# Optimization experiments

Hardware: AMD Instinct MI355X
Metric: run time of the kernel (lower is better)

## Reference

```python
import jax, jax.numpy as jnp
import numpy as np

N_NODES = 50000
N_EDGES = 600000
BAG = 16
VOCAB = 10000
EMB = 128
HID = 128
N_CLASSES = 10
N_GRAPHS = 512
PAD_IDX = 1


def setup_inputs() -> dict:
    key = jax.random.key(0)
    ks = jax.random.split(key, 12)
    x_tokens = jax.random.randint(ks[0], (N_NODES, BAG), 0, VOCAB)
    src = jax.random.randint(ks[1], (N_EDGES,), 0, N_NODES)
    dst = jax.random.randint(ks[2], (N_EDGES,), 0, N_NODES)
    edge_index = jnp.stack([src, dst])
    batch = jnp.sort(jax.random.randint(ks[3], (N_NODES,), 0, N_GRAPHS))
    # rows 0,1 are zero in the original (weights[2:] filled from pretrained vectors)
    emb_table = (jax.random.normal(ks[4], (VOCAB, EMB)) * 0.02).at[:2].set(0.0)
    s = 1.0 / np.sqrt(EMB)
    w1_l = jax.random.normal(ks[5], (HID, EMB)) * s
    b1 = jnp.zeros((HID,), jnp.float32)
    w1_r = jax.random.normal(ks[6], (HID, EMB)) * s
    w2_l = jax.random.normal(ks[7], (HID, HID)) * s
    b2 = jnp.zeros((HID,), jnp.float32)
    w2_r = jax.random.normal(ks[8], (HID, HID)) * s
    w_out = jax.random.normal(ks[9], (N_CLASSES, HID)) * s
    b_out = jnp.zeros((N_CLASSES,), jnp.float32)
    return {"x_tokens": x_tokens, "edge_index": edge_index, "batch": batch,
            "emb_table": emb_table, "w1_l": w1_l, "b1": b1, "w1_r": w1_r,
            "w2_l": w2_l, "b2": b2, "w2_r": w2_r, "w_out": w_out, "b_out": b_out}


def _embedding_bag_mean(tokens, table):
    # nn.EmbeddingBag mode='mean' with padding_idx: padding tokens excluded from mean
    emb = table[tokens]                                  # [N, BAG, D]
    mask = (tokens != PAD_IDX)[..., None].astype(table.dtype)
    total = jnp.sum(emb * mask, axis=1)                  # [N, D]
    cnt = jnp.clip(jnp.sum(mask, axis=1), 1.0)           # [N, 1]
    return total / cnt


def _sage_conv(x, src, dst, w_l, b_l, w_r):
    # PyG SAGEConv: lin_l(mean_{j in N(i)} x_j) + lin_r(x_i); lin_r has no bias
    n = x.shape[0]
    msg_sum = jax.ops.segment_sum(x[src], dst, num_segments=n)           # [N, D]
    deg = jax.ops.segment_sum(jnp.ones((src.shape[0], 1), x.dtype), dst,
                              num_segments=n)                             # [N, 1]
    aggr = msg_sum / jnp.clip(deg, 1.0)
    return aggr @ w_l.T + b_l + x @ w_r.T


def reference(x_tokens, edge_index, batch, emb_table, w1_l, b1, w1_r,
              w2_l, b2, w2_r, w_out, b_out):
    src, dst = edge_index[0], edge_index[1]
    x = _embedding_bag_mean(x_tokens, emb_table)                 # [N, EMB]
    x = jax.nn.relu(_sage_conv(x, src, dst, w1_l, b1, w1_r))     # [N, HID]
    x = jax.nn.relu(_sage_conv(x, src, dst, w2_l, b2, w2_r))     # [N, HID]
    # global_mean_pool over graph ids
    g_sum = jax.ops.segment_sum(x, batch, num_segments=N_GRAPHS)
    g_cnt = jax.ops.segment_sum(jnp.ones((x.shape[0], 1), x.dtype), batch,
                                num_segments=N_GRAPHS)
    g = g_sum / jnp.clip(g_cnt, 1.0)                             # [G, HID]
    return g @ w_out.T + b_out                                   # [G, C]
```

## Files before the change

### kernel.cpp

```cpp
#include <hip/hip_runtime.h>
#include <hip/hip_bf16.h>

#define NN 50000
#define NE 600000
#define BAG 16
#define EMB 128
#define HID 128
#define NC 10
#define NG 512
#define PAD_IDX 1
#define VOCAB 10000
#define SLOTS 64
#define TPAIRS (VOCAB * EMB / 2)
#define WPAIRS (4 * HID * EMB / 2)
#define NE8 (NE / 8)
#define SC8BLK ((NE8 + 255) / 256)
#define EMVB (NN / 16)
#define NTILES ((NN + 127) / 128)

typedef __attribute__((ext_vector_type(8))) short v8s;
typedef __attribute__((ext_vector_type(4))) float v4f;

__device__ __forceinline__ float bflo(unsigned u) { return __uint_as_float(u << 16); }
__device__ __forceinline__ float bfhi(unsigned u) { return __uint_as_float(u & 0xffff0000u); }
__device__ __forceinline__ unsigned short f2bf(float f) {
    unsigned u = __float_as_uint(f);
    return (unsigned short)((u + 0x7fffu + ((u >> 16) & 1u)) >> 16);
}
__device__ __forceinline__ void acc8(float* a, v8s v) {
    unsigned* u = (unsigned*)&v;
#pragma unroll
    for (int j = 0; j < 4; j++) {
        a[2 * j] += bflo(u[j]);
        a[2 * j + 1] += bfhi(u[j]);
    }
}

__global__ void k_conv(const float* __restrict__ t, unsigned short* __restrict__ tb,
                       const float* __restrict__ w1l, const float* __restrict__ w1r,
                       const float* __restrict__ w2l, const float* __restrict__ w2r,
                       unsigned short* __restrict__ wbf, int* __restrict__ cnt,
                       float* __restrict__ gsum, float* __restrict__ gcnt) {
    int i = blockIdx.x * blockDim.x + threadIdx.x;
    if (i < NN) cnt[i] = 0;
    if (i < NG * HID) gsum[i] = 0.f;
    if (i < NG) gcnt[i] = 0.f;
    if (i < TPAIRS) {
        float2 v = *(const float2*)(t + (size_t)i * 2);
        unsigned lo = f2bf(v.x), hi = f2bf(v.y);
        *(unsigned*)(tb + (size_t)i * 2) = lo | (hi << 16);
    } else if (i < TPAIRS + WPAIRS) {
        int j = i - TPAIRS;
        int k = j * 2;
        int arr = k >> 14;
        int o = k & 16383;
        const float* w = (arr == 0) ? w1l : (arr == 1) ? w1r : (arr == 2) ? w2l : w2r;
        float2 v = *(const float2*)(w + o);
        unsigned lo = f2bf(v.x), hi = f2bf(v.y);
        *(unsigned*)(wbf + k) = lo | (hi << 16);
    }
}

__global__ __launch_bounds__(256) void k_scatem(const int* __restrict__ src,
                                                const int* __restrict__ dst,
                                                int* __restrict__ cnt,
                                                int* __restrict__ slots,
                                                const int* __restrict__ tokens,
                                                const unsigned short* __restrict__ table,
                                                unsigned short* __restrict__ x0) {
    int b = blockIdx.x;
    if (b < EMVB) {
        int sl = threadIdx.x & 15;
        int node = b * 16 + (threadIdx.x >> 4);
        const int* tp = tokens + node * BAG;
        float a[8];
#pragma unroll
        for (int j = 0; j < 8; j++) a[j] = 0.f;
        int c = 0;
#pragma unroll
        for (int t = 0; t < BAG; t++) {
            int tok = tp[t];
            c += (tok != PAD_IDX);
            v8s v = *(const v8s*)(table + (size_t)tok * EMB + sl * 8);
            acc8(a, v);
        }
        float inv = 1.0f / (float)(c > 0 ? c : 1);
        uint4 o;
        o.x = f2bf(a[0] * inv) | ((unsigned)f2bf(a[1] * inv) << 16);
        o.y = f2bf(a[2] * inv) | ((unsigned)f2bf(a[3] * inv) << 16);
        o.z = f2bf(a[4] * inv) | ((unsigned)f2bf(a[5] * inv) << 16);
        o.w = f2bf(a[6] * inv) | ((unsigned)f2bf(a[7] * inv) << 16);
        *(uint4*)(x0 + (size_t)node * EMB + sl * 8) = o;
        return;
    }
    int t = (b - EMVB) * 256 + threadIdx.x;
    if (t < NE8) {
        int4 s0 = *((const int4*)src + t * 2);
        int4 s1 = *((const int4*)src + t * 2 + 1);
        int4 d0 = *((const int4*)dst + t * 2);
        int4 d1 = *((const int4*)dst + t * 2 + 1);
        int p0 = atomicAdd(&cnt[d0.x], 1);
        int p1 = atomicAdd(&cnt[d0.y], 1);
        int p2 = atomicAdd(&cnt[d0.z], 1);
        int p3 = atomicAdd(&cnt[d0.w], 1);
        int p4 = atomicAdd(&cnt[d1.x], 1);
        int p5 = atomicAdd(&cnt[d1.y], 1);
        int p6 = atomicAdd(&cnt[d1.z], 1);
        int p7 = atomicAdd(&cnt[d1.w], 1);
        if (p0 < SLOTS) slots[(size_t)d0.x * SLOTS + p0] = s0.x;
        if (p1 < SLOTS) slots[(size_t)d0.y * SLOTS + p1] = s0.y;
        if (p2 < SLOTS) slots[(size_t)d0.z * SLOTS + p2] = s0.z;
        if (p3 < SLOTS) slots[(size_t)d0.w * SLOTS + p3] = s0.w;
        if (p4 < SLOTS) slots[(size_t)d1.x * SLOTS + p4] = s1.x;
        if (p5 < SLOTS) slots[(size_t)d1.y * SLOTS + p5] = s1.y;
        if (p6 < SLOTS) slots[(size_t)d1.z * SLOTS + p6] = s1.z;
        if (p7 < SLOTS) slots[(size_t)d1.w * SLOTS + p7] = s1.w;
    }
}

__global__ __launch_bounds__(256) void k_aggr(const unsigned short* __restrict__ x,
                                              const int* __restrict__ cnt,
                                              const int* __restrict__ slots,
                                              unsigned short* __restrict__ aggr) {
    int node = blockIdx.x * 4 + (threadIdx.x >> 6);
    int lane = threadIdx.x & 63;
    if (node >= NN) return;
    int deg = cnt[node];
    int m = deg > SLOTS ? SLOTS : deg;
    int g = lane >> 4, sl = lane & 15;
    float a[8];
#pragma unroll
    for (int j = 0; j < 8; j++) a[j] = 0.f;
    int idx_l = slots[(size_t)node * SLOTS + ((lane < m) ? lane : 0)];
    int i = 0;
    for (; i + 8 <= m; i += 8) {
        int t0 = __shfl(idx_l, i + g, 64);
        int t1 = __shfl(idx_l, i + 4 + g, 64);
        v8s v0 = *(const v8s*)(x + (size_t)t0 * HID + sl * 8);
        v8s v1 = *(const v8s*)(x + (size_t)t1 * HID + sl * 8);
        acc8(a, v0);
        acc8(a, v1);
    }
    for (; i + 4 <= m; i += 4) {
        int t0 = __shfl(idx_l, i + g, 64);
        v8s v0 = *(const v8s*)(x + (size_t)t0 * HID + sl * 8);
        acc8(a, v0);
    }
    int rem = m - i;
    if (rem > 0) {
        int t0 = __shfl(idx_l, (g < rem) ? i + g : i, 64);
        v8s v0 = *(const v8s*)(x + (size_t)t0 * HID + sl * 8);
        if (g < rem) acc8(a, v0);
    }
#pragma unroll
    for (int j = 0; j < 8; j++) {
        a[j] += __shfl_xor(a[j], 16, 64);
        a[j] += __shfl_xor(a[j], 32, 64);
    }
    float inv = 1.0f / (float)(deg > 0 ? deg : 1);
    if (g == 0) {
        uint4 o;
        o.x = f2bf(a[0] * inv) | ((unsigned)f2bf(a[1] * inv) << 16);
        o.y = f2bf(a[2] * inv) | ((unsigned)f2bf(a[3] * inv) << 16);
        o.z = f2bf(a[4] * inv) | ((unsigned)f2bf(a[5] * inv) << 16);
        o.w = f2bf(a[6] * inv) | ((unsigned)f2bf(a[7] * inv) << 16);
        *(uint4*)(aggr + (size_t)node * HID + sl * 8) = o;
    }
}

__device__ __forceinline__ void sage_kloop(int row0, const unsigned short* __restrict__ xa,
                                           const unsigned short* __restrict__ xr,
                                           const unsigned short* __restrict__ wl,
                                           const unsigned short* __restrict__ wr,
                                           unsigned short* As, unsigned short* Bs,
                                           v4f acc[2][8]) {
    int tid = threadIdx.x;
    int wave = tid >> 6, lane = tid & 63;
    int q = lane >> 4, l16 = lane & 15;
    for (int kc = 0; kc < 8; kc++) {
        const unsigned short* Ag = (kc < 4) ? xa : xr;
        const unsigned short* Bg = (kc < 4) ? wl : wr;
        int koff = (kc & 3) * 32;
#pragma unroll
        for (int it = 0; it < 2; it++) {
            int seg = tid + it * 256;
            int r = seg >> 2, sg = seg & 3;
            int gr = row0 + r;
            if (gr > NN - 1) gr = NN - 1;
            v8s a = *(const v8s*)(Ag + (size_t)gr * HID + koff + sg * 8);
            *(v8s*)(As + r * 32 + sg * 8) = a;
            v8s b = *(const v8s*)(Bg + (size_t)r * HID + koff + sg * 8);
            *(v8s*)(Bs + r * 32 + sg * 8) = b;
        }
        __syncthreads();
        v8s a0 = *(const v8s*)(As + (wave * 32 + l16) * 32 + q * 8);
        v8s a1 = *(const v8s*)(As + (wave * 32 + 16 + l16) * 32 + q * 8);
#pragma unroll
        for (int nt = 0; nt < 8; nt++) {
            v8s b = *(const v8s*)(Bs + (nt * 16 + l16) * 32 + q * 8);
            acc[0][nt] = __builtin_amdgcn_mfma_f32_16x16x32_bf16(a0, b, acc[0][nt], 0, 0, 0);
            acc[1][nt] = __builtin_amdgcn_mfma_f32_16x16x32_bf16(a1, b, acc[1][nt], 0, 0, 0);
        }
        __syncthreads();
    }
}

__global__ __launch_bounds__(256) void k_sage(const unsigned short* __restrict__ xa,
                                              const unsigned short* __restrict__ xr,
                                              const unsigned short* __restrict__ wl,
                                              const unsigned short* __restrict__ wr,
                                              const float* __restrict__ bias,
                                              unsigned short* __restrict__ out) {
    __shared__ unsigned short As[128 * 32];
    __shared__ unsigned short Bs[128 * 32];
    int row0 = blockIdx.x * 128;
    v4f acc[2][8];
#pragma unroll
    for (int m = 0; m < 2; m++)
#pragma unroll
        for (int n = 0; n < 8; n++) acc[m][n] = (v4f){0.f, 0.f, 0.f, 0.f};
    sage_kloop(row0, xa, xr, wl, wr, As, Bs, acc);
    int tid = threadIdx.x;
    int wave = tid >> 6, lane = tid & 63;
    int q = lane >> 4, l16 = lane & 15;
#pragma unroll
    for (int nt = 0; nt < 8; nt++) {
        int col = nt * 16 + l16;
        float bv = bias[col];
#pragma unroll
        for (int mt = 0; mt < 2; mt++) {
#pragma unroll
            for (int r = 0; r < 4; r++) {
                int row = row0 + wave * 32 + mt * 16 + q * 4 + r;
                if (row < NN) {
                    float v = acc[mt][nt][r] + bv;
                    v = v > 0.f ? v : 0.f;
                    out[(size_t)row * HID + col] = f2bf(v);
                }
            }
        }
    }
}

__global__ __launch_bounds__(256) void k_sagepool(const unsigned short* __restrict__ xa,
                                                  const unsigned short* __restrict__ xr,
                                                  const unsigned short* __restrict__ wl,
                                                  const unsigned short* __restrict__ wr,
                                                  const float* __restrict__ bias,
                                                  const int* __restrict__ batch,
                                                  float* __restrict__ gsum,
                                                  float* __restrict__ gcnt) {
    __shared__ unsigned short smem[128 * 128];
    unsigned short* As = smem;
    unsigned short* Bs = smem + 128 * 32;
    int row0 = blockIdx.x * 128;
    v4f acc[2][8];
#pragma unroll
    for (int m = 0; m < 2; m++)
#pragma unroll
        for (int n = 0; n < 8; n++) acc[m][n] = (v4f){0.f, 0.f, 0.f, 0.f};
    sage_kloop(row0, xa, xr, wl, wr, As, Bs, acc);
    int tid = threadIdx.x;
    int wave = tid >> 6, lane = tid & 63;
    int q = lane >> 4, l16 = lane & 15;
#pragma unroll
    for (int nt = 0; nt < 8; nt++) {
        int col = nt * 16 + l16;
        float bv = bias[col];
#pragma unroll
        for (int mt = 0; mt < 2; mt++) {
#pragma unroll
            for (int r = 0; r < 4; r++) {
                int rl = wave * 32 + mt * 16 + q * 4 + r;
                float v = acc[mt][nt][r] + bv;
                v = v > 0.f ? v : 0.f;
                smem[rl * 128 + col] = f2bf(v);
            }
        }
    }
    __syncthreads();
    if (tid < 128) {
        int col = tid;
        int end = NN - row0;
        if (end > 128) end = 128;
        int cur = batch[row0];
        float acc_p = 0.f;
        int c = 0;
        for (int i = 0; i < end; i++) {
            int b = batch[row0 + i];
            if (b != cur) {
                atomicAdd(&gsum[cur * HID + col], acc_p);
                if (col == 0) atomicAdd(&gcnt[cur], (float)c);
                acc_p = 0.f;
                c = 0;
                cur = b;
            }
            acc_p += __uint_as_float(((unsigned)smem[i * 128 + col]) << 16);
            c++;
        }
        atomicAdd(&gsum[cur * HID + col], acc_p);
        if (col == 0) atomicAdd(&gcnt[cur], (float)c);
    }
}

__global__ __launch_bounds__(128) void k_final(const float* __restrict__ gsum,
                                               const float* __restrict__ gcnt,
                                               const float* __restrict__ w_out,
                                               const float* __restrict__ b_out,
                                               float* __restrict__ out) {
    __shared__ float mean[HID];
    int g = blockIdx.x, tid = threadIdx.x;
    mean[tid] = gsum[g * HID + tid] / fmaxf(gcnt[g], 1.0f);
    __syncthreads();
    if (tid < NC) {
        float s = b_out[tid];
#pragma unroll 16
        for (int d = 0; d < HID; d++) s += mean[d] * w_out[tid * HID + d];
        out[g * NC + tid] = s;
    }
}

extern "C" void kernel_launch(void* const* d_in, const int* in_sizes, int n_in,
                              void* d_out, int out_size, void* d_ws, size_t ws_size,
                              hipStream_t stream) {
    const int* x_tokens = (const int*)d_in[0];
    const int* edge = (const int*)d_in[1];
    const int* batch = (const int*)d_in[2];
    const float* emb_table = (const float*)d_in[3];
    const float* w1l = (const float*)d_in[4];
    const float* b1 = (const float*)d_in[5];
    const float* w1r = (const float*)d_in[6];
    const float* w2l = (const float*)d_in[7];
    const float* b2 = (const float*)d_in[8];
    const float* w2r = (const float*)d_in[9];
    const float* w_out = (const float*)d_in[10];
    const float* b_out = (const float*)d_in[11];
    float* out = (float*)d_out;

    char* ws = (char*)d_ws;
    size_t off = 0;
    auto alloc = [&](size_t bytes) {
        void* p = ws + off;
        off += (bytes + 255) & ~(size_t)255;
        return p;
    };
    int* cnt = (int*)alloc(NN * 4);
    int* slots = (int*)alloc((size_t)NN * SLOTS * 4);
    unsigned short* wbf = (unsigned short*)alloc(4 * HID * EMB * 2);
    float* gsum = (float*)alloc(NG * HID * 4);
    float* gcnt = (float*)alloc(NG * 4);
    unsigned short* x0 = (unsigned short*)alloc((size_t)NN * EMB * 2);
    unsigned short* x1 = (unsigned short*)alloc((size_t)NN * HID * 2);
    unsigned short* aggrb = (unsigned short*)alloc((size_t)NN * HID * 2);
    unsigned short* table_bf = x1;

    const int* srcp = edge;
    const int* dstp = edge + NE;

    k_conv<<<(TPAIRS + WPAIRS + 255) / 256, 256, 0, stream>>>(
        emb_table, table_bf, w1l, w1r, w2l, w2r, wbf, cnt, gsum, gcnt);
    k_scatem<<<EMVB + SC8BLK, 256, 0, stream>>>(srcp, dstp, cnt, slots, x_tokens,
                                                table_bf, x0);
    k_aggr<<<(NN + 3) / 4, 256, 0, stream>>>(x0, cnt, slots, aggrb);
    k_sage<<<NTILES, 256, 0, stream>>>(aggrb, x0, wbf, wbf + 16384, b1, x1);
    k_aggr<<<(NN + 3) / 4, 256, 0, stream>>>(x1, cnt, slots, aggrb);
    k_sagepool<<<NTILES, 256, 0, stream>>>(aggrb, x1, wbf + 32768, wbf + 49152, b2,
                                           batch, gsum, gcnt);
    k_final<<<NG, 128, 0, stream>>>(gsum, gcnt, w_out, b_out, out);
}
```

Before: 210.7 us.

## Assign 16 threads per node in aggregation instead of a full wave

The neighbor-mean aggregation kernel now maps each node to a 16-lane group, so one 256-thread block handles 16 nodes instead of 4. Each group walks its node's full neighbor list with vectorized int4 index loads and eight independent row gathers per iteration. This removes the cross-group shuffle reduction, the shuffle-based index broadcast and the idle lanes on low-degree nodes. In exchange, lanes within a wave can diverge when node degrees differ, and each thread serially accumulates more rows.

Measured after the change: 213.5 us. Within noise of the previous version (+1.3%).

```diff
diff --git a/kernel.cpp b/kernel.cpp
--- a/kernel.cpp
+++ b/kernel.cpp
@@ -16,6 +16,7 @@
 #define NE8 (NE / 8)
 #define SC8BLK ((NE8 + 255) / 256)
 #define EMVB (NN / 16)
+#define AGVB (NN / 16)
 #define NTILES ((NN + 127) / 128)
 
 typedef __attribute__((ext_vector_type(8))) short v8s;
@@ -122,50 +123,58 @@
                                               const int* __restrict__ cnt,
                                               const int* __restrict__ slots,
                                               unsigned short* __restrict__ aggr) {
-    int node = blockIdx.x * 4 + (threadIdx.x >> 6);
-    int lane = threadIdx.x & 63;
-    if (node >= NN) return;
+    int sl = threadIdx.x & 15;
+    int node = blockIdx.x * 16 + (threadIdx.x >> 4);
     int deg = cnt[node];
     int m = deg > SLOTS ? SLOTS : deg;
-    int g = lane >> 4, sl = lane & 15;
+    const int* srow = slots + (size_t)node * SLOTS;
     float a[8];
 #pragma unroll
     for (int j = 0; j < 8; j++) a[j] = 0.f;
-    int idx_l = slots[(size_t)node * SLOTS + ((lane < m) ? lane : 0)];
-    int i = 0;
-    for (; i + 8 <= m; i += 8) {
-        int t0 = __shfl(idx_l, i + g, 64);
-        int t1 = __shfl(idx_l, i + 4 + g, 64);
-        v8s v0 = *(const v8s*)(x + (size_t)t0 * HID + sl * 8);
-        v8s v1 = *(const v8s*)(x + (size_t)t1 * HID + sl * 8);
+    int t = 0;
+    for (; t + 8 <= m; t += 8) {
+        int4 i0 = *(const int4*)(srow + t);
+        int4 i1 = *(const int4*)(srow + t + 4);
+        v8s v0 = *(const v8s*)(x + (size_t)i0.x * HID + sl * 8);
+        v8s v1 = *(const v8s*)(x + (size_t)i0.y * HID + sl * 8);
+        v8s v2 = *(const v8s*)(x + (size_t)i0.z * HID + sl * 8);
+        v8s v3 = *(const v8s*)(x + (size_t)i0.w * HID + sl * 8);
+        v8s v4 = *(const v8s*)(x + (size_t)i1.x * HID + sl * 8);
+        v8s v5 = *(const v8s*)(x + (size_t)i1.y * HID + sl * 8);
+        v8s v6 = *(const v8s*)(x + (size_t)i1.z * HID + sl * 8);
+        v8s v7 = *(const v8s*)(x + (size_t)i1.w * HID + sl * 8);
         acc8(a, v0);
         acc8(a, v1);
-    }
-    for (; i + 4 <= m; i += 4) {
-        int t0 = __shfl(idx_l, i + g, 64);
-        v8s v0 = *(const v8s*)(x + (size_t)t0 * HID + sl * 8);
+        acc8(a, v2);
+        acc8(a, v3);
+        acc8(a, v4);
+        acc8(a, v5);
+        acc8(a, v6);
+        acc8(a, v7);
+    }
+    for (; t + 4 <= m; t += 4) {
+        int4 id = *(const int4*)(srow + t);
+        v8s v0 = *(const v8s*)(x + (size_t)id.x * HID + sl * 8);
+        v8s v1 = *(const v8s*)(x + (size_t)id.y * HID + sl * 8);
+        v8s v2 = *(const v8s*)(x + (size_t)id.z * HID + sl * 8);
+        v8s v3 = *(const v8s*)(x + (size_t)id.w * HID + sl * 8);
         acc8(a, v0);
-    }
-    int rem = m - i;
-    if (rem > 0) {
-        int t0 = __shfl(idx_l, (g < rem) ? i + g : i, 64);
-        v8s v0 = *(const v8s*)(x + (size_t)t0 * HID + sl * 8);
-        if (g < rem) acc8(a, v0);
-    }
-#pragma unroll
-    for (int j = 0; j < 8; j++) {
-        a[j] += __shfl_xor(a[j], 16, 64);
-        a[j] += __shfl_xor(a[j], 32, 64);
+        acc8(a, v1);
+        acc8(a, v2);
+        acc8(a, v3);
+    }
+    for (; t < m; t++) {
+        int id = srow[t];
+        v8s v = *(const v8s*)(x + (size_t)id * HID + sl * 8);
+        acc8(a, v);
     }
     float inv = 1.0f / (float)(deg > 0 ? deg : 1);
-    if (g == 0) {
-        uint4 o;
-        o.x = f2bf(a[0] * inv) | ((unsigned)f2bf(a[1] * inv) << 16);
-        o.y = f2bf(a[2] * inv) | ((unsigned)f2bf(a[3] * inv) << 16);
-        o.z = f2bf(a[4] * inv) | ((unsigned)f2bf(a[5] * inv) << 16);
-        o.w = f2bf(a[6] * inv) | ((unsigned)f2bf(a[7] * inv) << 16);
-        *(uint4*)(aggr + (size_t)node * HID + sl * 8) = o;
-    }
+    uint4 o;
+    o.x = f2bf(a[0] * inv) | ((unsigned)f2bf(a[1] * inv) << 16);
+    o.y = f2bf(a[2] * inv) | ((unsigned)f2bf(a[3] * inv) << 16);
+    o.z = f2bf(a[4] * inv) | ((unsigned)f2bf(a[5] * inv) << 16);
+    o.w = f2bf(a[6] * inv) | ((unsigned)f2bf(a[7] * inv) << 16);
+    *(uint4*)(aggr + (size_t)node * HID + sl * 8) = o;
 }
 
 __device__ __forceinline__ void sage_kloop(int row0, const unsigned short* __restrict__ xa,
@@ -361,9 +370,9 @@
         emb_table, table_bf, w1l, w1r, w2l, w2r, wbf, cnt, gsum, gcnt);
     k_scatem<<<EMVB + SC8BLK, 256, 0, stream>>>(srcp, dstp, cnt, slots, x_tokens,
                                                 table_bf, x0);
-    k_aggr<<<(NN + 3) / 4, 256, 0, stream>>>(x0, cnt, slots, aggrb);
+    k_aggr<<<AGVB, 256, 0, stream>>>(x0, cnt, slots, aggrb);
     k_sage<<<NTILES, 256, 0, stream>>>(aggrb, x0, wbf, wbf + 16384, b1, x1);
-    k_aggr<<<(NN + 3) / 4, 256, 0, stream>>>(x1, cnt, slots, aggrb);
+    k_aggr<<<AGVB, 256, 0, stream>>>(x1, cnt, slots, aggrb);
     k_sagepool<<<NTILES, 256, 0, stream>>>(aggrb, x1, wbf + 32768, wbf + 49152, b2,
                                            batch, gsum, gcnt);
     k_final<<<NG, 128, 0, stream>>>(gsum, gcnt, w_out, b_out, out);
```
